# Optimization experiments

Measured on AMD Instinct MI355X. Metric: run time of the kernel, lower is better.

## Reference

```python
import jax, jax.numpy as jnp
import numpy as np

D_MODEL = 1024
N_HEADS = 16
HEAD_DIM = D_MODEL // N_HEADS
B, LQ, LK = 4, 2048, 2048


def _rope(x, cos, sin):
    # x: (B, H, L, d); cos/sin: (B, 1, L, d)
    d = x.shape[-1]
    x1, x2 = x[..., : d // 2], x[..., d // 2 :]
    rotated = jnp.concatenate([-x2, x1], axis=-1)
    return x * cos + rotated * sin


def setup_inputs() -> dict:
    key = jax.random.key(0)
    ks = jax.random.split(key, 16)
    s = 1.0 / np.sqrt(D_MODEL)
    inp = {
        "query": jax.random.normal(ks[0], (B, LQ, D_MODEL), jnp.float32),
        "key": jax.random.normal(ks[1], (B, LK, D_MODEL), jnp.float32),
        "value": jax.random.normal(ks[2], (B, LK, D_MODEL), jnp.float32),
        "cos_q": jax.random.normal(ks[3], (B, LQ, HEAD_DIM), jnp.float32),
        "sin_q": jax.random.normal(ks[4], (B, LQ, HEAD_DIM), jnp.float32),
        "cos_k": jax.random.normal(ks[5], (B, LK, HEAD_DIM), jnp.float32),
        "sin_k": jax.random.normal(ks[6], (B, LK, HEAD_DIM), jnp.float32),
        "key_padding_mask": jnp.zeros((B, LK), dtype=bool),
        "Wq": jax.random.normal(ks[7], (D_MODEL, D_MODEL), jnp.float32) * s,
        "bq": jnp.zeros((D_MODEL,), jnp.float32),
        "Wk": jax.random.normal(ks[8], (D_MODEL, D_MODEL), jnp.float32) * s,
        "bk": jnp.zeros((D_MODEL,), jnp.float32),
        "Wv": jax.random.normal(ks[9], (D_MODEL, D_MODEL), jnp.float32) * s,
        "bv": jnp.zeros((D_MODEL,), jnp.float32),
        "Wo": jax.random.normal(ks[10], (D_MODEL, D_MODEL), jnp.float32) * s,
        "bo": jnp.zeros((D_MODEL,), jnp.float32),
    }
    return inp


def reference(query, key, value, cos_q, sin_q, cos_k, sin_k, key_padding_mask,
              Wq, bq, Wk, bk, Wv, bv, Wo, bo):
    Bq, Lq, _ = query.shape
    Lk = key.shape[1]
    scale = HEAD_DIM ** -0.5

    def proj(x, W, b, L):
        # torch Linear: x @ W.T + b, then (B, L, H, d) -> (B, H, L, d)
        y = jnp.einsum('ble,de->bld', x, W) + b
        return y.reshape(Bq, L, N_HEADS, HEAD_DIM).transpose(0, 2, 1, 3)

    q = proj(query, Wq, bq, Lq)
    k = proj(key, Wk, bk, Lk)
    v = proj(value, Wv, bv, Lk)

    q = _rope(q, cos_q[:, None, :Lq, :HEAD_DIM], sin_q[:, None, :Lq, :HEAD_DIM])
    k = _rope(k, cos_k[:, None, :Lk, :HEAD_DIM], sin_k[:, None, :Lk, :HEAD_DIM])

    attn = jnp.einsum('bhqd,bhkd->bhqk', q, k) * scale
    attn = jnp.where(key_padding_mask[:, None, None, :], -jnp.inf, attn)
    attn = jax.nn.softmax(attn, axis=-1)

    out = jnp.einsum('bhqk,bhkd->bhqd', attn, v)
    out = out.transpose(0, 2, 1, 3).reshape(Bq, Lq, D_MODEL)
    return jnp.einsum('ble,de->bld', out, Wo) + bo
```

## Files before the change

### kernel.cpp

```cpp
#include <hip/hip_runtime.h>
#include <hip/hip_bf16.h>
#include <stdint.h>
#include <stddef.h>

#define B_DIM 4
#define NH    16
#define LSEQ  2048
#define HD    64
#define DM    1024
#define TOKENS (B_DIM * LSEQ)

typedef __bf16 bf16_t;
typedef __attribute__((ext_vector_type(8))) __bf16 bf16x8;
typedef __attribute__((ext_vector_type(4))) __bf16 bf16x4;
typedef __attribute__((ext_vector_type(4))) float  f32x4;

#define GLD16(gp, lp) \
  __builtin_amdgcn_global_load_lds((__attribute__((address_space(1))) void*)(gp), \
                                   (__attribute__((address_space(3))) void*)(lp), 16, 0, 0)

#define WAITV8 asm volatile("s_waitcnt vmcnt(8)" ::: "memory")
#define WAITV4 asm volatile("s_waitcnt vmcnt(4)" ::: "memory")
#define WAITV0 asm volatile("s_waitcnt vmcnt(0)" ::: "memory")
#define WAITL0 asm volatile("s_waitcnt lgkmcnt(0)" ::: "memory")
#define SBAR   __builtin_amdgcn_s_barrier()
#define SCHED0 __builtin_amdgcn_sched_barrier(0)

__device__ __forceinline__ f32x4 mfma_16x16x32(bf16x8 a, bf16x8 b, f32x4 c) {
  return __builtin_amdgcn_mfma_f32_16x16x32_bf16(a, b, c, 0, 0, 0);
}

__global__ __launch_bounds__(256) void cast3_kernel(const float* __restrict__ a,
                                                    const float* __restrict__ b,
                                                    const float* __restrict__ c,
                                                    bf16_t* __restrict__ dst, int n) {
  const float* src = (blockIdx.y == 0) ? a : (blockIdx.y == 1) ? b : c;
  const int i = (blockIdx.x * 256 + threadIdx.x) * 4;
  if (i < n) {
    const float4 v = *(const float4*)(src + i);
    bf16x4 o;
    o[0] = (bf16_t)v.x; o[1] = (bf16_t)v.y; o[2] = (bf16_t)v.z; o[3] = (bf16_t)v.w;
    *(bf16x4*)(dst + (size_t)blockIdx.y * n + i) = o;
  }
}

__global__ __launch_bounds__(256) void cast4_kernel(const float* __restrict__ a,
                                                    const float* __restrict__ b,
                                                    const float* __restrict__ c,
                                                    const float* __restrict__ d,
                                                    bf16_t* __restrict__ dst, int n) {
  const float* src = (blockIdx.y == 0) ? a : (blockIdx.y == 1) ? b
                   : (blockIdx.y == 2) ? c : d;
  const int i = (blockIdx.x * 256 + threadIdx.x) * 4;
  if (i < n) {
    const float4 v = *(const float4*)(src + i);
    bf16x4 o;
    o[0] = (bf16_t)v.x; o[1] = (bf16_t)v.y; o[2] = (bf16_t)v.z; o[3] = (bf16_t)v.w;
    *(bf16x4*)(dst + (size_t)blockIdx.y * n + i) = o;
  }
}

#define GEMM_TILE(CUR, WAIT, PRE, KK2)                                        \
  {                                                                           \
    WAIT; SBAR; SCHED0;                                                       \
    const bf16_t* Ac = &As[CUR][0];                                           \
    const bf16_t* Bc = &Bs[CUR][0];                                           \
    bf16x8 af[4], bfr[4];                                                     \
    _Pragma("unroll") for (int i_ = 0; i_ < 4; ++i_)                          \
      af[i_] = *(const bf16x8*)(Ac + (wm + i_ * 16 + l16) * 32 + fcol);       \
    _Pragma("unroll") for (int j_ = 0; j_ < 4; ++j_)                          \
      bfr[j_] = *(const bf16x8*)(Bc + (wn + j_ * 16 + l16) * 32 + fcol);      \
    _Pragma("unroll") for (int i_ = 0; i_ < 4; ++i_)                          \
      _Pragma("unroll") for (int j_ = 0; j_ < 4; ++j_)                        \
        acc[i_][j_] = mfma_16x16x32(af[i_], bfr[j_], acc[i_][j_]);            \
    WAITL0; SBAR; SCHED0;                                                     \
    if (PRE) {                                                                \
      const int kk2_ = (KK2);                                                 \
      GLD16(Ag0 + kk2_, &As[CUR][0] + ld0);                                   \
      GLD16(Ag1 + kk2_, &As[CUR][0] + ld1);                                   \
      GLD16(Bg0 + kk2_, &Bs[CUR][0] + ld0);                                   \
      GLD16(Bg1 + kk2_, &Bs[CUR][0] + ld1);                                   \
    }                                                                         \
  }

#define GEMM_LOOP                                                             \
  GLD16(Ag0, &As[0][0] + ld0); GLD16(Ag1, &As[0][0] + ld1);                   \
  GLD16(Bg0, &Bs[0][0] + ld0); GLD16(Bg1, &Bs[0][0] + ld1);                   \
  GLD16(Ag0 + 32, &As[1][0] + ld0); GLD16(Ag1 + 32, &As[1][0] + ld1);         \
  GLD16(Bg0 + 32, &Bs[1][0] + ld0); GLD16(Bg1 + 32, &Bs[1][0] + ld1);         \
  GLD16(Ag0 + 64, &As[2][0] + ld0); GLD16(Ag1 + 64, &As[2][0] + ld1);         \
  GLD16(Bg0 + 64, &Bs[2][0] + ld0); GLD16(Bg1 + 64, &Bs[2][0] + ld1);         \
  for (int ii = 0; ii < 9; ++ii) {                                            \
    const int kkb = ii * 96 + 96;                                             \
    GEMM_TILE(0, WAITV8, true, kkb);                                          \
    GEMM_TILE(1, WAITV8, true, kkb + 32);                                     \
    GEMM_TILE(2, WAITV8, true, kkb + 64);                                     \
  }                                                                           \
  GEMM_TILE(0, WAITV8, true, 960);                                            \
  GEMM_TILE(1, WAITV8, true, 992);                                            \
  GEMM_TILE(2, WAITV8, false, 0);                                             \
  GEMM_TILE(0, WAITV4, false, 0);                                             \
  GEMM_TILE(1, WAITV0, false, 0);

__global__ __launch_bounds__(256) void qkv_proj_kernel(const bf16_t* __restrict__ X,
                                                       const bf16_t* __restrict__ Wb,
                                                       const float* __restrict__ bq,
                                                       const float* __restrict__ bk,
                                                       const float* __restrict__ bv,
                                                       const float* __restrict__ cos_q,
                                                       const float* __restrict__ sin_q,
                                                       const float* __restrict__ cos_k,
                                                       const float* __restrict__ sin_k,
                                                       bf16_t* __restrict__ qtb,
                                                       bf16_t* __restrict__ ktb,
                                                       bf16_t* __restrict__ vtb) {
  __shared__ bf16_t As[3][128 * 32];
  __shared__ bf16_t Bs[3][128 * 32];
  const int z = blockIdx.z;
  const bf16_t* A  = X  + (size_t)z * TOKENS * DM;
  const bf16_t* Bw = Wb + (size_t)z * DM * DM;
  const float* bias = (z == 0) ? bq : (z == 1) ? bk : bv;

  const int tid  = threadIdx.x;
  const int wave = tid >> 6, lane = tid & 63;
  const int quad = lane >> 4, l16 = lane & 15;
  const int L  = blockIdx.x + (blockIdx.y << 6);
  const int mt = ((L & 7) << 3) | ((L >> 3) & 7);
  const int nt = L >> 6;
  const int m0 = mt * 128, n0 = nt * 128;
  const int wm = (wave >> 1) * 64, wn = (wave & 1) * 64;

  f32x4 acc[4][4];
#pragma unroll
  for (int i = 0; i < 4; ++i)
#pragma unroll
    for (int j = 0; j < 4; ++j) acc[i][j] = (f32x4){0.f, 0.f, 0.f, 0.f};

  const int srow = lane >> 2;
  const int scol = ((lane & 3) ^ ((lane >> 3) & 3)) * 8;
  const int c0 = wave * 2, c1 = c0 + 1;
  const int r0 = c0 * 16 + srow, r1 = c1 * 16 + srow;
  const bf16_t* Ag0 = A  + (size_t)(m0 + r0) * DM + scol;
  const bf16_t* Ag1 = A  + (size_t)(m0 + r1) * DM + scol;
  const bf16_t* Bg0 = Bw + (size_t)(n0 + r0) * DM + scol;
  const bf16_t* Bg1 = Bw + (size_t)(n0 + r1) * DM + scol;
  const int ld0 = c0 * 512, ld1 = c1 * 512;

  const int fcol = ((quad ^ ((l16 >> 1) & 3)) << 3);

  GEMM_LOOP

  if (z < 2) {
    const float* cosb = (z == 0) ? cos_q : cos_k;
    const float* sinb = (z == 0) ? sin_q : sin_k;
    bf16_t* out = (z == 0) ? qtb : ktb;
    const int h = (n0 + wn) >> 6;
#pragma unroll
    for (int i = 0; i < 4; ++i) {
#pragma unroll
      for (int j = 0; j < 2; ++j) {
        const int hd1 = j * 16 + l16;
        const int hd2 = hd1 + 32;
        const float bn1 = bias[n0 + wn + hd1];
        const float bn2 = bias[n0 + wn + hd2];
#pragma unroll
        for (int r = 0; r < 4; ++r) {
          const int m = m0 + wm + i * 16 + quad * 4 + r;
          const int b = m >> 11, l = m & (LSEQ - 1);
          const size_t cb = ((size_t)b * LSEQ + l) * HD;
          const float x1 = (float)(bf16_t)(acc[i][j][r] + bn1);
          const float x2 = (float)(bf16_t)(acc[i][j + 2][r] + bn2);
          const float c1 = cosb[cb + hd1], s1 = sinb[cb + hd1];
          const float c2 = cosb[cb + hd2], s2 = sinb[cb + hd2];
          bf16_t* dst = out + (((size_t)(b * NH + h)) * LSEQ + l) * HD;
          dst[hd1] = (bf16_t)(x1 * c1 - x2 * s1);
          dst[hd2] = (bf16_t)(x2 * c2 + x1 * s2);
        }
      }
    }
  } else {
#pragma unroll
    for (int i = 0; i < 4; ++i) {
      const int mb = m0 + wm + i * 16 + quad * 4;
      const int b = mb >> 11, l = mb & (LSEQ - 1);
#pragma unroll
      for (int j = 0; j < 4; ++j) {
        const int n = n0 + wn + j * 16 + l16;
        const int h = n >> 6, hd = n & (HD - 1);
        const float bn = bias[n];
        bf16x4 pk;
#pragma unroll
        for (int r = 0; r < 4; ++r) pk[r] = (bf16_t)(acc[i][j][r] + bn);
        *(bf16x4*)(vtb + (((size_t)(b * NH + h)) * HD + hd) * LSEQ + l) = pk;
      }
    }
  }
}

__global__ __launch_bounds__(256) void out_gemm_kernel(const bf16_t* __restrict__ A,
                                                       const bf16_t* __restrict__ Bw,
                                                       const float* __restrict__ bias,
                                                       float* __restrict__ out) {
  __shared__ bf16_t As[3][128 * 32];
  __shared__ bf16_t Bs[3][128 * 32];
  const int tid  = threadIdx.x;
  const int wave = tid >> 6, lane = tid & 63;
  const int quad = lane >> 4, l16 = lane & 15;
  const int L  = blockIdx.x + (blockIdx.y << 6);
  const int mt = ((L & 7) << 3) | ((L >> 3) & 7);
  const int nt = L >> 6;
  const int m0 = mt * 128, n0 = nt * 128;
  const int wm = (wave >> 1) * 64, wn = (wave & 1) * 64;

  f32x4 acc[4][4];
#pragma unroll
  for (int i = 0; i < 4; ++i)
#pragma unroll
    for (int j = 0; j < 4; ++j) acc[i][j] = (f32x4){0.f, 0.f, 0.f, 0.f};

  const int srow = lane >> 2;
  const int scol = ((lane & 3) ^ ((lane >> 3) & 3)) * 8;
  const int c0 = wave * 2, c1 = c0 + 1;
  const int r0 = c0 * 16 + srow, r1 = c1 * 16 + srow;
  const bf16_t* Ag0 = A  + (size_t)(m0 + r0) * DM + scol;
  const bf16_t* Ag1 = A  + (size_t)(m0 + r1) * DM + scol;
  const bf16_t* Bg0 = Bw + (size_t)(n0 + r0) * DM + scol;
  const bf16_t* Bg1 = Bw + (size_t)(n0 + r1) * DM + scol;
  const int ld0 = c0 * 512, ld1 = c1 * 512;
  const int fcol = ((quad ^ ((l16 >> 1) & 3)) << 3);

  GEMM_LOOP

#pragma unroll
  for (int i = 0; i < 4; ++i)
#pragma unroll
    for (int j = 0; j < 4; ++j) {
      const int n  = n0 + wn + j * 16 + l16;
      const float bn = bias[n];
#pragma unroll
      for (int r = 0; r < 4; ++r) {
        const int m = m0 + wm + i * 16 + quad * 4 + r;
        out[(size_t)m * DM + n] = acc[i][j][r] + bn;
      }
    }
}

#define ATTN_TILE(K0)                                                         \
  {                                                                           \
    const bf16_t* Kc = &Kl[cur][0];                                           \
    const bf16_t* Vc = &Vl[cur][0];                                           \
    f32x4 S[2][4];                                                            \
    _Pragma("unroll") for (int j = 0; j < 4; ++j) {                           \
      const bf16x8 kb0 = *(const bf16x8*)(Kc + oA + j * 1024);                \
      const bf16x8 kb1 = *(const bf16x8*)(Kc + oB + j * 1024);                \
      _Pragma("unroll") for (int u = 0; u < 2; ++u) {                         \
        f32x4 a = (f32x4){0.f, 0.f, 0.f, 0.f};                                \
        a = mfma_16x16x32(kb0, qa[u][0], a);                                  \
        a = mfma_16x16x32(kb1, qa[u][1], a);                                  \
        _Pragma("unroll") for (int r = 0; r < 4; ++r)                         \
          S[u][j][r] = __builtin_amdgcn_exp2f(a[r] * scale_l2e);              \
      }                                                                       \
    }                                                                         \
    if (has_mask) {                                                           \
      const uint64_t mlo = *(const uint64_t*)(mrow + (K0) + quad * 8);        \
      const uint64_t mhi = *(const uint64_t*)(mrow + (K0) + 32 + quad * 8);   \
      if (!__all((mlo | mhi) == 0)) {                                         \
        _Pragma("unroll") for (int j = 0; j < 4; ++j) {                       \
          const uint64_t mm = (j & 2) ? mhi : mlo;                            \
          _Pragma("unroll") for (int r = 0; r < 4; ++r)                       \
            if ((mm >> (((j & 1) * 4 + r) * 8)) & 0xff) {                     \
              S[0][j][r] = 0.f;                                               \
              S[1][j][r] = 0.f;                                               \
            }                                                                 \
        }                                                                     \
      }                                                                       \
    }                                                                         \
    bf16x8 pa[2][2];                                                          \
    _Pragma("unroll") for (int u = 0; u < 2; ++u)                             \
      _Pragma("unroll") for (int f = 0; f < 2; ++f)                           \
        _Pragma("unroll") for (int e = 0; e < 8; ++e)                         \
          pa[u][f][e] = (bf16_t)S[u][2 * f + (e >> 2)][e & 3];                \
    _Pragma("unroll") for (int u = 0; u < 2; ++u) {                           \
      Ol[u] = mfma_16x16x32(pa[u][0], ones, Ol[u]);                           \
      Ol[u] = mfma_16x16x32(pa[u][1], ones, Ol[u]);                           \
    }                                                                         \
    _Pragma("unroll") for (int jd = 0; jd < 4; ++jd) {                        \
      const bf16x8 vb0 = *(const bf16x8*)(Vc + oA + jd * 1024);               \
      const bf16x8 vb1 = *(const bf16x8*)(Vc + oB + jd * 1024);               \
      _Pragma("unroll") for (int u = 0; u < 2; ++u) {                         \
        O[u][jd] = mfma_16x16x32(pa[u][0], vb0, O[u][jd]);                    \
        O[u][jd] = mfma_16x16x32(pa[u][1], vb1, O[u][jd]);                    \
      }                                                                       \
    }                                                                         \
  }

__global__ __launch_bounds__(256, 4) void attn_kernel(const bf16_t* __restrict__ qt,
                                                      const bf16_t* __restrict__ kt,
                                                      const bf16_t* __restrict__ vt,
                                                      const unsigned char* __restrict__ mask,
                                                      bf16_t* __restrict__ ctx) {
  __shared__ bf16_t Kl[2][64 * 64];
  __shared__ bf16_t Vl[2][64 * 64];
  __shared__ int mflag;
  const int L  = blockIdx.x + (blockIdx.y << 4);
  const int bh = ((L & 7) << 3) | ((L >> 3) & 7);
  const int q0 = (L >> 6) * 128;
  const int b = bh >> 4, h = bh & (NH - 1);
  const int tid = threadIdx.x;
  const int wave = tid >> 6, lane = tid & 63;
  const int quad = lane >> 4, l16 = lane & 15;
  const float scale_l2e = 0.125f * 1.44269504f;

  const bf16_t* kbase = kt + (size_t)bh * LSEQ * HD;
  const bf16_t* vbase = vt + (size_t)bh * HD * LSEQ;
  const unsigned char* mrow = mask + (size_t)b * LSEQ;

  if (tid == 0) mflag = 0;
  __syncthreads();
  {
    const uint64_t mw = ((const uint64_t*)mrow)[tid];
    if (mw != 0) atomicOr(&mflag, 1);
  }

  bf16x8 qa[2][2];
#pragma unroll
  for (int u = 0; u < 2; ++u) {
    const bf16_t* qrow = qt + (((size_t)bh * LSEQ) + q0 + wave * 32 + u * 16 + l16) * HD;
    qa[u][0] = *(const bf16x8*)(qrow + quad * 8);
    qa[u][1] = *(const bf16x8*)(qrow + 32 + quad * 8);
  }

  f32x4 O[2][4];
  f32x4 Ol[2];
#pragma unroll
  for (int u = 0; u < 2; ++u) {
    Ol[u] = (f32x4){0.f, 0.f, 0.f, 0.f};
#pragma unroll
    for (int j = 0; j < 4; ++j) O[u][j] = (f32x4){0.f, 0.f, 0.f, 0.f};
  }
  bf16x8 ones;
#pragma unroll
  for (int e = 0; e < 8; ++e) ones[e] = (bf16_t)1.0f;

  const int srow8 = lane >> 3;
  const int scb   = lane & 7;
  const int c0 = wave * 2, c1 = c0 + 1;
  const int p0 = c0 * 8 + srow8, p1 = p0 + 8;
  const int g0 = (scb ^ srow8) * 8;
  const int sig0 = ((p0 >> 5) << 5) | (((p0 >> 2) & 3) << 3) | (((p0 >> 4) & 1) << 2) | (p0 & 3);
  const int sig1 = ((p1 >> 5) << 5) | (((p1 >> 2) & 3) << 3) | (((p1 >> 4) & 1) << 2) | (p1 & 3);
  const int kgo0 = sig0 * HD + g0, kgo1 = sig1 * HD + g0;
  const int vgo0 = p0 * LSEQ + g0, vgo1 = p1 * LSEQ + g0;
  const int ld0 = c0 * 512, ld1 = c1 * 512;

  const int sw  = l16 & 7;
  const int oA  = l16 * 64 + ((quad ^ sw) << 3);
  const int oB  = l16 * 64 + (((quad + 4) ^ sw) << 3);

  GLD16(kbase + kgo0, &Kl[0][0] + ld0);
  GLD16(kbase + kgo1, &Kl[0][0] + ld1);
  GLD16(vbase + vgo0, &Vl[0][0] + ld0);
  GLD16(vbase + vgo1, &Vl[0][0] + ld1);
  GLD16(kbase + (size_t)64 * HD + kgo0, &Kl[1][0] + ld0);
  GLD16(kbase + (size_t)64 * HD + kgo1, &Kl[1][0] + ld1);
  GLD16(vbase + (size_t)(vgo0 + 64), &Vl[1][0] + ld0);
  GLD16(vbase + (size_t)(vgo1 + 64), &Vl[1][0] + ld1);

  WAITL0; SBAR;
  const bool has_mask = (mflag != 0);

  int cur = 0;
  for (int t = 0; t < 30; ++t) {
    WAITV4; SBAR; SCHED0;
    ATTN_TILE(t * 64);
    WAITL0; SBAR; SCHED0;
    {
      const int k0n = t * 64 + 128;
      bf16_t* Kd = &Kl[cur][0];
      bf16_t* Vd = &Vl[cur][0];
      GLD16(kbase + (size_t)k0n * HD + kgo0, Kd + ld0);
      GLD16(kbase + (size_t)k0n * HD + kgo1, Kd + ld1);
      GLD16(vbase + (size_t)(vgo0 + k0n), Vd + ld0);
      GLD16(vbase + (size_t)(vgo1 + k0n), Vd + ld1);
    }
    cur ^= 1;
  }
  WAITV4; SBAR; SCHED0;
  ATTN_TILE(30 * 64);
  cur ^= 1;
  WAITV0; SBAR; SCHED0;
  ATTN_TILE(31 * 64);

#pragma unroll
  for (int u = 0; u < 2; ++u) {
    f32x4 linv;
#pragma unroll
    for (int r = 0; r < 4; ++r) linv[r] = 1.0f / Ol[u][r];
#pragma unroll
    for (int jd = 0; jd < 4; ++jd)
#pragma unroll
      for (int r = 0; r < 4; ++r) {
        const int l = q0 + wave * 32 + u * 16 + quad * 4 + r;
        const int d = h * HD + jd * 16 + l16;
        const float o = O[u][jd][r] * linv[r];
        ctx[((size_t)b * LSEQ + l) * DM + d] = (bf16_t)o;
      }
  }
}

extern "C" void kernel_launch(void* const* d_in, const int* in_sizes, int n_in,
                              void* d_out, int out_size, void* d_ws, size_t ws_size,
                              hipStream_t stream) {
  (void)in_sizes; (void)n_in; (void)out_size; (void)ws_size;
  const float* query = (const float*)d_in[0];
  const float* key   = (const float*)d_in[1];
  const float* value = (const float*)d_in[2];
  const float* cos_q = (const float*)d_in[3];
  const float* sin_q = (const float*)d_in[4];
  const float* cos_k = (const float*)d_in[5];
  const float* sin_k = (const float*)d_in[6];
  const unsigned char* mask = (const unsigned char*)d_in[7];
  const float* Wq = (const float*)d_in[8];
  const float* bq = (const float*)d_in[9];
  const float* Wk = (const float*)d_in[10];
  const float* bk = (const float*)d_in[11];
  const float* Wv = (const float*)d_in[12];
  const float* bv = (const float*)d_in[13];
  const float* Wo = (const float*)d_in[14];
  const float* bo = (const float*)d_in[15];
  float* out = (float*)d_out;

  const size_t ACT = (size_t)TOKENS * DM;
  const size_t WEL = (size_t)DM * DM;

  bf16_t* p   = (bf16_t*)d_ws;
  bf16_t* xq  = p; p += ACT;
  bf16_t* xk  = p; p += ACT;
  bf16_t* xv  = p; p += ACT;
  bf16_t* wqb = p; p += WEL;
  bf16_t* wkb = p; p += WEL;
  bf16_t* wvb = p; p += WEL;
  bf16_t* wob = p; p += WEL;
  bf16_t* qtb = p; p += ACT;
  bf16_t* ktb = p; p += ACT;
  bf16_t* vtb = p; p += ACT;
  bf16_t* ctx = xk;
  (void)xv; (void)wkb; (void)wvb;

  cast3_kernel<<<dim3((int)(ACT / 1024), 3), 256, 0, stream>>>(query, key, value, xq, (int)ACT);
  cast4_kernel<<<dim3((int)(WEL / 1024), 4), 256, 0, stream>>>(Wq, Wk, Wv, Wo, wqb, (int)WEL);

  qkv_proj_kernel<<<dim3(TOKENS / 128, DM / 128, 3), 256, 0, stream>>>(
      xq, wqb, bq, bk, bv, cos_q, sin_q, cos_k, sin_k, qtb, ktb, vtb);

  attn_kernel<<<dim3(LSEQ / 128, B_DIM * NH), 256, 0, stream>>>(qtb, ktb, vtb, mask, ctx);

  out_gemm_kernel<<<dim3(TOKENS / 128, DM / 128), 256, 0, stream>>>(ctx, wob, bo, out);
}
```

Measured before the change: 363.8 us.

## Merge cast kernels, interleave cos/sin, double-buffer GEMMs, drop tile swizzle

Folds the two fp32-to-bf16 cast kernels into one prep kernel that also interleaves cos and sin into float2 pairs, stored temporarily in the output buffer, so the RoPE epilogue does one 8-byte load per element instead of two. The GEMM pipeline goes from triple to double buffering of the LDS tiles, with a shallower vmcnt wait, which cuts LDS use per block. The grouped block-to-tile swizzle is replaced by plain row-major block indexing. Together these save a launch and some epilogue loads, but risk more exposed load latency and worse L2 locality in the GEMMs.

```diff
diff --git a/kernel.cpp b/kernel.cpp
--- a/kernel.cpp
+++ b/kernel.cpp
@@ -19,7 +19,6 @@
   __builtin_amdgcn_global_load_lds((__attribute__((address_space(1))) void*)(gp), \
                                    (__attribute__((address_space(3))) void*)(lp), 16, 0, 0)
 
-#define WAITV8 asm volatile("s_waitcnt vmcnt(8)" ::: "memory")
 #define WAITV4 asm volatile("s_waitcnt vmcnt(4)" ::: "memory")
 #define WAITV0 asm volatile("s_waitcnt vmcnt(0)" ::: "memory")
 #define WAITL0 asm volatile("s_waitcnt lgkmcnt(0)" ::: "memory")
@@ -30,33 +29,50 @@
   return __builtin_amdgcn_mfma_f32_16x16x32_bf16(a, b, c, 0, 0, 0);
 }
 
-__global__ __launch_bounds__(256) void cast3_kernel(const float* __restrict__ a,
-                                                    const float* __restrict__ b,
-                                                    const float* __restrict__ c,
-                                                    bf16_t* __restrict__ dst, int n) {
-  const float* src = (blockIdx.y == 0) ? a : (blockIdx.y == 1) ? b : c;
-  const int i = (blockIdx.x * 256 + threadIdx.x) * 4;
-  if (i < n) {
-    const float4 v = *(const float4*)(src + i);
+__global__ __launch_bounds__(256) void prep_kernel(const float* __restrict__ q,
+                                                   const float* __restrict__ k,
+                                                   const float* __restrict__ v,
+                                                   const float* __restrict__ Wq,
+                                                   const float* __restrict__ Wk,
+                                                   const float* __restrict__ Wv,
+                                                   const float* __restrict__ Wo,
+                                                   const float* __restrict__ cos_q,
+                                                   const float* __restrict__ sin_q,
+                                                   const float* __restrict__ cos_k,
+                                                   const float* __restrict__ sin_k,
+                                                   bf16_t* __restrict__ xdst,
+                                                   bf16_t* __restrict__ wdst,
+                                                   float2* __restrict__ cs) {
+  const int bid = blockIdx.x;
+  const int tid = threadIdx.x;
+  if (bid < 24576) {
+    const int s = bid >> 13, off = bid & 8191;
+    const float* src = (s == 0) ? q : (s == 1) ? k : v;
+    const int i = (off * 256 + tid) * 4;
+    const float4 val = *(const float4*)(src + i);
     bf16x4 o;
-    o[0] = (bf16_t)v.x; o[1] = (bf16_t)v.y; o[2] = (bf16_t)v.z; o[3] = (bf16_t)v.w;
-    *(bf16x4*)(dst + (size_t)blockIdx.y * n + i) = o;
-  }
-}
-
-__global__ __launch_bounds__(256) void cast4_kernel(const float* __restrict__ a,
-                                                    const float* __restrict__ b,
-                                                    const float* __restrict__ c,
-                                                    const float* __restrict__ d,
-                                                    bf16_t* __restrict__ dst, int n) {
-  const float* src = (blockIdx.y == 0) ? a : (blockIdx.y == 1) ? b
-                   : (blockIdx.y == 2) ? c : d;
-  const int i = (blockIdx.x * 256 + threadIdx.x) * 4;
-  if (i < n) {
-    const float4 v = *(const float4*)(src + i);
+    o[0] = (bf16_t)val.x; o[1] = (bf16_t)val.y; o[2] = (bf16_t)val.z; o[3] = (bf16_t)val.w;
+    *(bf16x4*)(xdst + (size_t)s * (TOKENS * (size_t)DM) + i) = o;
+  } else if (bid < 28672) {
+    const int s = (bid - 24576) >> 10, off = (bid - 24576) & 1023;
+    const float* src = (s == 0) ? Wq : (s == 1) ? Wk : (s == 2) ? Wv : Wo;
+    const int i = (off * 256 + tid) * 4;
+    const float4 val = *(const float4*)(src + i);
     bf16x4 o;
-    o[0] = (bf16_t)v.x; o[1] = (bf16_t)v.y; o[2] = (bf16_t)v.z; o[3] = (bf16_t)v.w;
-    *(bf16x4*)(dst + (size_t)blockIdx.y * n + i) = o;
+    o[0] = (bf16_t)val.x; o[1] = (bf16_t)val.y; o[2] = (bf16_t)val.z; o[3] = (bf16_t)val.w;
+    *(bf16x4*)(wdst + (size_t)s * (DM * (size_t)DM) + i) = o;
+  } else {
+    const int s = (bid - 28672) >> 9, off = (bid - 28672) & 511;
+    const float* cp = (s == 0) ? cos_q : cos_k;
+    const float* sp = (s == 0) ? sin_q : sin_k;
+    const int i = (off * 256 + tid) * 4;
+    const float4 c4 = *(const float4*)(cp + i);
+    const float4 s4 = *(const float4*)(sp + i);
+    float2* d = cs + (size_t)s * (TOKENS * (size_t)HD) + i;
+    d[0] = make_float2(c4.x, s4.x);
+    d[1] = make_float2(c4.y, s4.y);
+    d[2] = make_float2(c4.z, s4.z);
+    d[3] = make_float2(c4.w, s4.w);
   }
 }
 
@@ -88,17 +104,11 @@
   GLD16(Bg0, &Bs[0][0] + ld0); GLD16(Bg1, &Bs[0][0] + ld1);                   \
   GLD16(Ag0 + 32, &As[1][0] + ld0); GLD16(Ag1 + 32, &As[1][0] + ld1);         \
   GLD16(Bg0 + 32, &Bs[1][0] + ld0); GLD16(Bg1 + 32, &Bs[1][0] + ld1);         \
-  GLD16(Ag0 + 64, &As[2][0] + ld0); GLD16(Ag1 + 64, &As[2][0] + ld1);         \
-  GLD16(Bg0 + 64, &Bs[2][0] + ld0); GLD16(Bg1 + 64, &Bs[2][0] + ld1);         \
-  for (int ii = 0; ii < 9; ++ii) {                                            \
-    const int kkb = ii * 96 + 96;                                             \
-    GEMM_TILE(0, WAITV8, true, kkb);                                          \
-    GEMM_TILE(1, WAITV8, true, kkb + 32);                                     \
-    GEMM_TILE(2, WAITV8, true, kkb + 64);                                     \
+  for (int ii = 0; ii < 15; ++ii) {                                           \
+    const int kk2a = ii * 64 + 64;                                            \
+    GEMM_TILE(0, WAITV4, true, kk2a);                                         \
+    GEMM_TILE(1, WAITV4, true, kk2a + 32);                                    \
   }                                                                           \
-  GEMM_TILE(0, WAITV8, true, 960);                                            \
-  GEMM_TILE(1, WAITV8, true, 992);                                            \
-  GEMM_TILE(2, WAITV8, false, 0);                                             \
   GEMM_TILE(0, WAITV4, false, 0);                                             \
   GEMM_TILE(1, WAITV0, false, 0);
 
@@ -107,15 +117,13 @@
                                                        const float* __restrict__ bq,
                                                        const float* __restrict__ bk,
                                                        const float* __restrict__ bv,
-                                                       const float* __restrict__ cos_q,
-                                                       const float* __restrict__ sin_q,
-                                                       const float* __restrict__ cos_k,
-                                                       const float* __restrict__ sin_k,
+                                                       const float2* __restrict__ csq,
+                                                       const float2* __restrict__ csk,
                                                        bf16_t* __restrict__ qtb,
                                                        bf16_t* __restrict__ ktb,
                                                        bf16_t* __restrict__ vtb) {
-  __shared__ bf16_t As[3][128 * 32];
-  __shared__ bf16_t Bs[3][128 * 32];
+  __shared__ bf16_t As[2][128 * 32];
+  __shared__ bf16_t Bs[2][128 * 32];
   const int z = blockIdx.z;
   const bf16_t* A  = X  + (size_t)z * TOKENS * DM;
   const bf16_t* Bw = Wb + (size_t)z * DM * DM;
@@ -124,10 +132,7 @@
   const int tid  = threadIdx.x;
   const int wave = tid >> 6, lane = tid & 63;
   const int quad = lane >> 4, l16 = lane & 15;
-  const int L  = blockIdx.x + (blockIdx.y << 6);
-  const int mt = ((L & 7) << 3) | ((L >> 3) & 7);
-  const int nt = L >> 6;
-  const int m0 = mt * 128, n0 = nt * 128;
+  const int m0 = blockIdx.x * 128, n0 = blockIdx.y * 128;
   const int wm = (wave >> 1) * 64, wn = (wave & 1) * 64;
 
   f32x4 acc[4][4];
@@ -151,8 +156,7 @@
   GEMM_LOOP
 
   if (z < 2) {
-    const float* cosb = (z == 0) ? cos_q : cos_k;
-    const float* sinb = (z == 0) ? sin_q : sin_k;
+    const float2* cst = (z == 0) ? csq : csk;
     bf16_t* out = (z == 0) ? qtb : ktb;
     const int h = (n0 + wn) >> 6;
 #pragma unroll
@@ -170,11 +174,11 @@
           const size_t cb = ((size_t)b * LSEQ + l) * HD;
           const float x1 = (float)(bf16_t)(acc[i][j][r] + bn1);
           const float x2 = (float)(bf16_t)(acc[i][j + 2][r] + bn2);
-          const float c1 = cosb[cb + hd1], s1 = sinb[cb + hd1];
-          const float c2 = cosb[cb + hd2], s2 = sinb[cb + hd2];
+          const float2 cs1 = cst[cb + hd1];
+          const float2 cs2 = cst[cb + hd2];
           bf16_t* dst = out + (((size_t)(b * NH + h)) * LSEQ + l) * HD;
-          dst[hd1] = (bf16_t)(x1 * c1 - x2 * s1);
-          dst[hd2] = (bf16_t)(x2 * c2 + x1 * s2);
+          dst[hd1] = (bf16_t)(x1 * cs1.x - x2 * cs1.y);
+          dst[hd2] = (bf16_t)(x2 * cs2.x + x1 * cs2.y);
         }
       }
     }
@@ -201,15 +205,12 @@
                                                        const bf16_t* __restrict__ Bw,
                                                        const float* __restrict__ bias,
                                                        float* __restrict__ out) {
-  __shared__ bf16_t As[3][128 * 32];
-  __shared__ bf16_t Bs[3][128 * 32];
+  __shared__ bf16_t As[2][128 * 32];
+  __shared__ bf16_t Bs[2][128 * 32];
   const int tid  = threadIdx.x;
   const int wave = tid >> 6, lane = tid & 63;
   const int quad = lane >> 4, l16 = lane & 15;
-  const int L  = blockIdx.x + (blockIdx.y << 6);
-  const int mt = ((L & 7) << 3) | ((L >> 3) & 7);
-  const int nt = L >> 6;
-  const int m0 = mt * 128, n0 = nt * 128;
+  const int m0 = blockIdx.x * 128, n0 = blockIdx.y * 128;
   const int wm = (wave >> 1) * 64, wn = (wave & 1) * 64;
 
   f32x4 acc[4][4];
@@ -432,6 +433,7 @@
 
   const size_t ACT = (size_t)TOKENS * DM;
   const size_t WEL = (size_t)DM * DM;
+  const size_t CSN = (size_t)TOKENS * HD;
 
   bf16_t* p   = (bf16_t*)d_ws;
   bf16_t* xq  = p; p += ACT;
@@ -447,11 +449,15 @@
   bf16_t* ctx = xk;
   (void)xv; (void)wkb; (void)wvb;
 
-  cast3_kernel<<<dim3((int)(ACT / 1024), 3), 256, 0, stream>>>(query, key, value, xq, (int)ACT);
-  cast4_kernel<<<dim3((int)(WEL / 1024), 4), 256, 0, stream>>>(Wq, Wk, Wv, Wo, wqb, (int)WEL);
+  float2* csq = (float2*)out;
+  float2* csk = csq + CSN;
+
+  prep_kernel<<<dim3(29696), 256, 0, stream>>>(query, key, value, Wq, Wk, Wv, Wo,
+                                               cos_q, sin_q, cos_k, sin_k,
+                                               xq, wqb, csq);
 
   qkv_proj_kernel<<<dim3(TOKENS / 128, DM / 128, 3), 256, 0, stream>>>(
-      xq, wqb, bq, bk, bv, cos_q, sin_q, cos_k, sin_k, qtb, ktb, vtb);
+      xq, wqb, bq, bk, bv, csq, csk, qtb, ktb, vtb);
 
   attn_kernel<<<dim3(LSEQ / 128, B_DIM * NH), 256, 0, stream>>>(qtb, ktb, vtb, mask, ctx);
 
```

New measurement: 355.1 us. 2.4% less time.
